# Optimization experiments

Hardware: AMD Instinct MI355X
Metric: run time of the kernel (lower is better)

## Reference

```python
import jax, jax.numpy as jnp
import numpy as np

EPS = 1e-5

def _conv_bn_relu(x, w, gamma, beta):
    # x: [B, C, N], w: [O, C] (1x1 conv, no bias)
    y = jnp.einsum('oc,bcn->bon', w, x)
    # BatchNorm1d in training mode: per-channel stats over (B, N)
    mean = jnp.mean(y, axis=(0, 2), keepdims=True)
    var = jnp.var(y, axis=(0, 2), keepdims=True)
    yhat = (y - mean) * jax.lax.rsqrt(var + EPS)
    return jax.nn.relu(gamma[None, :, None] * yhat + beta[None, :, None])


def setup_inputs() -> dict:
    key = jax.random.key(0)
    ks = jax.random.split(key, 8)
    B, C, N, Cr = 4, 256, 4096, 32
    x = jax.random.normal(ks[0], (B, C, N), dtype=jnp.float32)
    w1 = jax.random.normal(ks[1], (Cr, C), dtype=jnp.float32) * (1.0 / np.sqrt(C))
    w2 = jax.random.normal(ks[2], (Cr, C), dtype=jnp.float32) * (1.0 / np.sqrt(C))
    w3 = jax.random.normal(ks[3], (C, C), dtype=jnp.float32) * (1.0 / np.sqrt(C))
    g1 = 1.0 + 0.1 * jax.random.normal(ks[4], (Cr,), dtype=jnp.float32)
    b1 = 0.1 * jax.random.normal(ks[5], (Cr,), dtype=jnp.float32)
    g2 = 1.0 + 0.1 * jax.random.normal(ks[6], (Cr,), dtype=jnp.float32)
    b2 = 0.1 * jax.random.normal(ks[7], (Cr,), dtype=jnp.float32)
    g3 = jnp.ones((C,), dtype=jnp.float32)
    b3 = jnp.zeros((C,), dtype=jnp.float32)
    return {'x': x, 'w1': w1, 'w2': w2, 'w3': w3,
            'g1': g1, 'b1': b1, 'g2': g2, 'b2': b2, 'g3': g3, 'b3': b3}


def reference(x, w1, w2, w3, g1, b1, g2, b2, g3, b3):
    # a: [B, N, Cr] (queries), k: [B, Cr, N] (keys)
    a = _conv_bn_relu(x, w1, g1, b1).transpose(0, 2, 1)
    k = _conv_bn_relu(x, w2, g2, b2)
    # s[b, n, m] = softmax_m(sum_c a[b,n,c] * k[b,c,m])
    s = jax.nn.softmax(jnp.einsum('bnc,bcm->bnm', a, k), axis=-1)
    d = _conv_bn_relu(x, w3, g3, b3)  # [B, C, N]
    # out = x + d @ s^T : out[b,c,m] = sum_n d[b,c,n] * s[m,n]
    out = x + jnp.einsum('bcn,bmn->bcm', d, s)
    return out
```

## Files before the change

### kernel.cpp

```cpp
#include <hip/hip_runtime.h>
#include <cstddef>
#include <cstdint>

#define B_ 4
#define C_ 256
#define N_ 4096
#define KF_OFF_B  ((size_t)1024 * 1024)
#define DF_OFF_B  ((size_t)2 * 1024 * 1024)
#define SUM_OFF_B ((size_t)10 * 1024 * 1024)
#define ML_OFF_B  (SUM_OFF_B + 1280 * 4)
#define XH_OFF_B  (ML_OFF_B + 524288)
#define XL_OFF_B  (XH_OFF_B + (size_t)8 * 1024 * 1024)
#define WH_OFF_B  (XL_OFF_B + (size_t)8 * 1024 * 1024)
#define WL_OFF_B  (WH_OFF_B + 163840)
#define LOG2E 1.4426950408889634f

typedef unsigned short bfraw;
typedef __attribute__((ext_vector_type(8))) short short8;
typedef __attribute__((ext_vector_type(4))) float float4v;
typedef __attribute__((ext_vector_type(4))) bfraw bfraw4;

__device__ inline bfraw f2bf(float f) {
    union { float f; uint32_t u; } c; c.f = f;
    uint32_t u = c.u;
    u += 0x7fffu + ((u >> 16) & 1u);
    return (bfraw)(u >> 16);
}
__device__ inline float bf2f(bfraw h) {
    union { uint32_t u; float f; } c; c.u = ((uint32_t)h) << 16;
    return c.f;
}
#if __has_builtin(__builtin_amdgcn_exp2f)
__device__ inline float EXP2(float x) { return __builtin_amdgcn_exp2f(x); }
#else
__device__ inline float EXP2(float x) { return exp2f(x); }
#endif
__device__ inline uint32_t pack2(float a, float b) {
    union { float f; uint32_t u; } ca, cb; ca.f = a; cb.f = b;
#if __has_builtin(__builtin_amdgcn_perm)
    return __builtin_amdgcn_perm(cb.u + 0x8000u, ca.u + 0x8000u, 0x07060302u);
#else
    return ((ca.u + 0x8000u) >> 16) | ((cb.u + 0x8000u) & 0xffff0000u);
#endif
}

__global__ __launch_bounds__(256) void prep_kernel(
    const float* __restrict__ x,
    const float* __restrict__ w1, const float* __restrict__ w2,
    const float* __restrict__ w3, uint8_t* __restrict__ wsb)
{
    __shared__ float Ls[64][65];
    if (blockIdx.x >= 1024) {
        int bid = blockIdx.x - 1024;
        if (bid == 0) {
            float* sums = (float*)(wsb + SUM_OFF_B);
            for (int i = threadIdx.x; i < 640; i += 256) sums[i] = 0.f;
        }
        bfraw* wh = (bfraw*)(wsb + WH_OFF_B);
        bfraw* wl = (bfraw*)(wsb + WL_OFF_B);
        int idx4 = (bid * 256 + threadIdx.x) * 4;
        int ch = idx4 >> 8, k = idx4 & 255;
        const float* wr = (ch < 32) ? (w1 + ch * C_)
                          : (ch < 64) ? (w2 + (ch - 32) * C_)
                                      : (w3 + (ch - 64) * C_);
        float4 v = *(const float4*)&wr[k];
        float va[4] = {v.x, v.y, v.z, v.w};
        bfraw4 h, l;
#pragma unroll
        for (int j = 0; j < 4; ++j) {
            h[j] = f2bf(va[j]);
            l[j] = f2bf(va[j] - bf2f(h[j]));
        }
        *(bfraw4*)&wh[idx4] = h;
        *(bfraw4*)&wl[idx4] = l;
        return;
    }
    bfraw* xh = (bfraw*)(wsb + XH_OFF_B);
    bfraw* xl = (bfraw*)(wsb + XL_OFF_B);
    const int id = blockIdx.x;
    const int b  = id >> 8;
    const int c0 = ((id >> 6) & 3) << 6;
    const int n0 = (id & 63) << 6;
    const int t  = threadIdx.x;
    {
        int cl = t >> 4, nc = (t & 15) << 2;
#pragma unroll
        for (int i = 0; i < 4; ++i) {
            float4 v = *(const float4*)&x[((size_t)b * C_ + c0 + cl + i * 16) * N_ + n0 + nc];
            Ls[cl + i * 16][nc + 0] = v.x;
            Ls[cl + i * 16][nc + 1] = v.y;
            Ls[cl + i * 16][nc + 2] = v.z;
            Ls[cl + i * 16][nc + 3] = v.w;
        }
    }
    __syncthreads();
    int nl = t >> 2, seg = t & 3;
    bfraw hb[16], lb[16];
#pragma unroll
    for (int j = 0; j < 16; ++j) {
        float v = Ls[seg * 16 + j][nl];
        bfraw h = f2bf(v);
        hb[j] = h;
        lb[j] = f2bf(v - bf2f(h));
    }
    size_t base = ((size_t)b * N_ + n0 + nl) * 256 + c0 + seg * 16;
    *(short8*)&xh[base]     = *(short8*)&hb[0];
    *(short8*)&xh[base + 8] = *(short8*)&hb[8];
    *(short8*)&xl[base]     = *(short8*)&lb[0];
    *(short8*)&xl[base + 8] = *(short8*)&lb[8];
}

__global__ __launch_bounds__(256, 2) void ygemm_kernel(uint8_t* __restrict__ wsb)
{
    const bfraw* xh = (const bfraw*)(wsb + XH_OFF_B);
    const bfraw* xl = (const bfraw*)(wsb + XL_OFF_B);
    const bfraw* wh = (const bfraw*)(wsb + WH_OFF_B);
    const bfraw* wl = (const bfraw*)(wsb + WL_OFF_B);
    bfraw* qf  = (bfraw*)wsb;
    bfraw* kfp = (bfraw*)(wsb + KF_OFF_B);
    bfraw* dfp = (bfraw*)(wsb + DF_OFF_B);
    float* sums  = (float*)(wsb + SUM_OFF_B);
    float* sumsq = sums + 320;
    __shared__ float redS[4][64], redQ[4][64];

    const int bx = blockIdx.x;
    const int by = blockIdx.y;
    const int b  = bx >> 5;
    const int n0 = (bx << 7) & (N_ - 1);
    const int t = threadIdx.x, w = t >> 6, l = t & 63, lq = l & 15, lg = l >> 4;
    const int nw = n0 + w * 32;

    float4v acc[4][2];
#pragma unroll
    for (int i = 0; i < 4; ++i)
#pragma unroll
        for (int j = 0; j < 2; ++j) acc[i][j] = (float4v){0.f, 0.f, 0.f, 0.f};

    for (int s = 0; s < 8; ++s) {
        const int k0 = s * 32;
        short8 ah[4], al[4], bh[2], bl[2];
#pragma unroll
        for (int ct = 0; ct < 4; ++ct) {
            size_t off = (size_t)(by * 64 + ct * 16 + lq) * 256 + k0 + lg * 8;
            ah[ct] = *(const short8*)&wh[off];
            al[ct] = *(const short8*)&wl[off];
        }
#pragma unroll
        for (int nt = 0; nt < 2; ++nt) {
            size_t off = ((size_t)b * N_ + nw + nt * 16 + lq) * 256 + k0 + lg * 8;
            bh[nt] = *(const short8*)&xh[off];
            bl[nt] = *(const short8*)&xl[off];
        }
#pragma unroll
        for (int ct = 0; ct < 4; ++ct)
#pragma unroll
            for (int nt = 0; nt < 2; ++nt) {
                acc[ct][nt] = __builtin_amdgcn_mfma_f32_16x16x32_bf16(ah[ct], bh[nt], acc[ct][nt], 0, 0, 0);
                acc[ct][nt] = __builtin_amdgcn_mfma_f32_16x16x32_bf16(al[ct], bh[nt], acc[ct][nt], 0, 0, 0);
                acc[ct][nt] = __builtin_amdgcn_mfma_f32_16x16x32_bf16(ah[ct], bl[nt], acc[ct][nt], 0, 0, 0);
            }
    }
#pragma unroll
    for (int ct = 0; ct < 4; ++ct) {
        float sv[4], qv[4];
#pragma unroll
        for (int r = 0; r < 4; ++r) {
            float a0 = acc[ct][0][r], a1 = acc[ct][1][r];
            sv[r] = a0 + a1;
            qv[r] = a0 * a0 + a1 * a1;
#pragma unroll
            for (int m = 1; m < 16; m <<= 1) {
                sv[r] += __shfl_xor(sv[r], m);
                qv[r] += __shfl_xor(qv[r], m);
            }
        }
        if (lq == 0) {
#pragma unroll
            for (int r = 0; r < 4; ++r) {
                redS[w][ct * 16 + lg * 4 + r] = sv[r];
                redQ[w][ct * 16 + lg * 4 + r] = qv[r];
            }
        }
    }
    __syncthreads();
    if (t < 64) {
        float s = redS[0][t] + redS[1][t] + redS[2][t] + redS[3][t];
        float q = redQ[0][t] + redQ[1][t] + redQ[2][t] + redQ[3][t];
        atomicAdd(&sums[by * 64 + t], s);
        atomicAdd(&sumsq[by * 64 + t], q);
    }
    if (by == 0) {
#pragma unroll
        for (int ct = 0; ct < 4; ++ct)
#pragma unroll
            for (int nt = 0; nt < 2; ++nt)
#pragma unroll
                for (int r = 0; r < 4; ++r) {
                    int c = ct * 16 + lg * 4 + r;
                    int n = nw + nt * 16 + lq;
                    size_t addr = ((size_t)(b << 8) + (n >> 4)) * 512
                                + (size_t)(((n & 15) | (((c >> 3) & 3) << 4)) << 3) + (c & 7);
                    bfraw v = f2bf(acc[ct][nt][r]);
                    if (c < 32) qf[addr] = v; else kfp[addr] = v;
                }
    } else {
#pragma unroll
        for (int ct = 0; ct < 4; ++ct)
#pragma unroll
            for (int nt = 0; nt < 2; ++nt)
#pragma unroll
                for (int r = 0; r < 4; ++r) {
                    int cg = (by - 1) * 64 + ct * 16 + lg * 4 + r;
                    int n = nw + nt * 16 + lq;
                    size_t addr = (((size_t)(b << 4) + (cg >> 4)) * 128 + (n >> 5)) * 512
                                + (size_t)(((cg & 15) | (((n >> 3) & 3) << 4)) << 3) + (n & 7);
                    dfp[addr] = f2bf(acc[ct][nt][r]);
                }
    }
}

__device__ inline void bn_coef(const float* __restrict__ sums,
                               const float* __restrict__ g1, const float* __restrict__ b1,
                               const float* __restrict__ g2, const float* __restrict__ b2,
                               const float* __restrict__ g3, const float* __restrict__ b3,
                               int ch, float& sc, float& bi)
{
    const float inv = 1.0f / (float)(B_ * N_);
    float mean = sums[ch] * inv;
    float var  = sums[320 + ch] * inv - mean * mean;
    float g, bb;
    if (ch < 32)      { g = g1[ch];      bb = b1[ch]; }
    else if (ch < 64) { g = g2[ch - 32]; bb = b2[ch - 32]; }
    else              { g = g3[ch - 64]; bb = b3[ch - 64]; }
    sc = g * rsqrtf(var + 1e-5f);
    bi = bb - sc * mean;
    if (ch < 32) { sc *= LOG2E; bi *= LOG2E; }
}

__global__ __launch_bounds__(256) void affine_kernel(
    uint8_t* __restrict__ wsb,
    const float* __restrict__ g1, const float* __restrict__ b1,
    const float* __restrict__ g2, const float* __restrict__ b2,
    const float* __restrict__ g3, const float* __restrict__ b3)
{
    bfraw* base = (bfraw*)wsb;
    const float* sums = (const float*)(wsb + SUM_OFF_B);
    size_t i8 = ((size_t)blockIdx.x * 256 + threadIdx.x) * 8;
    bfraw4 v0 = *(bfraw4*)&base[i8];
    bfraw4 v1 = *(bfraw4*)&base[i8 + 4];
    if (i8 < 1048576) {
        int ch0 = (((int)(i8 >> 7)) & 3) * 8 + ((i8 < 524288) ? 0 : 32);
        float sa[8], ca[8];
#pragma unroll
        for (int j = 0; j < 8; ++j)
            bn_coef(sums, g1, b1, g2, b2, g3, b3, ch0 + j, sa[j], ca[j]);
#pragma unroll
        for (int j = 0; j < 4; ++j) {
            v0[j] = f2bf(fmaxf(0.f, fmaf(sa[j],     bf2f(v0[j]), ca[j])));
            v1[j] = f2bf(fmaxf(0.f, fmaf(sa[j + 4], bf2f(v1[j]), ca[j + 4])));
        }
    } else {
        size_t rel = i8 - 1048576;
        int ch = 64 + (((int)(rel >> 16)) & 15) * 16 + (((int)(rel >> 3)) & 15);
        float s, b;
        bn_coef(sums, g1, b1, g2, b2, g3, b3, ch, s, b);
#pragma unroll
        for (int j = 0; j < 4; ++j) {
            v0[j] = f2bf(fmaxf(0.f, fmaf(s, bf2f(v0[j]), b)));
            v1[j] = f2bf(fmaxf(0.f, fmaf(s, bf2f(v1[j]), b)));
        }
    }
    *(bfraw4*)&base[i8] = v0;
    *(bfraw4*)&base[i8 + 4] = v1;
}

__global__ __launch_bounds__(512, 2) void flash_kernel(
    const float* __restrict__ x, const uint8_t* __restrict__ wsb,
    float* __restrict__ out)
{
    const bfraw* qf  = (const bfraw*)wsb;
    const bfraw* kfp = (const bfraw*)(wsb + KF_OFF_B);
    const bfraw* dfp = (const bfraw*)(wsb + DF_OFF_B);
    __shared__ bfraw Pl[2][64 * 128];
    __shared__ bfraw kst[2][8 * 512];
    __shared__ float mfac[2][2][64];
    __shared__ uint2 flagw[2];
    __shared__ float msh[2][64], lsh[2][64];

    const int id  = blockIdx.x;
    const int b   = id & 3;
    const int n0q = (id >> 2) << 6;
    const int tid = threadIdx.x;
    const int w   = tid >> 6;
    const int l   = tid & 63;
    const int lq  = l & 15;
    const int lg  = l >> 4;
    const int sw  = lq & 7;
    const int qt_s   = w >> 1;
    const int ks_loc = w & 1;
    const int ctg0 = w;
    const int ctg1 = 8 + w;

    const short8 qfrag = *(const short8*)&qf[((size_t)(b * 256 + (n0q >> 4) + qt_s)) * 512 + l * 8];

    float m = 0.f, ps = 0.f;
    float4v zv = {0.f, 0.f, 0.f, 0.f};

    float4v accA[2][4], accB[2][4];
#pragma unroll
    for (int i = 0; i < 2; ++i)
#pragma unroll
        for (int j = 0; j < 4; ++j) {
            accA[i][j] = (float4v){0.f, 0.f, 0.f, 0.f};
            accB[i][j] = (float4v){0.f, 0.f, 0.f, 0.f};
        }

    short8 dfr[2][4];
#pragma unroll
    for (int ch = 0; ch < 4; ++ch) {
        dfr[0][ch] = *(const short8*)&dfp[(((size_t)(b * 16 + ctg0)) * 128 + ch) * 512 + l * 8];
        dfr[1][ch] = *(const short8*)&dfp[(((size_t)(b * 16 + ctg1)) * 128 + ch) * 512 + l * 8];
    }
    {
        short8 v = *(const short8*)&kfp[((size_t)(b * 256 + w)) * 512 + l * 8];
        *(short8*)&kst[0][w * 512 + l * 8] = v;
    }
    __syncthreads();

    const int qrow = qt_s * 16 + lq;
    for (int it = 0; it < 32; ++it) {
        const int ib = it & 1;
        const int nit = (it + 1) & 31;
        short8 kstage = *(const short8*)&kfp[((size_t)(b * 256 + nit * 8 + w)) * 512 + l * 8];
        short8 kfr[4];
#pragma unroll
        for (int kt = 0; kt < 4; ++kt)
            kfr[kt] = *(const short8*)&kst[ib][(ks_loc * 4 + kt) * 512 + l * 8];
        float4v st[4];
#pragma unroll
        for (int kt = 0; kt < 4; ++kt)
            st[kt] = __builtin_amdgcn_mfma_f32_16x16x32_bf16(kfr[kt], qfrag, zv, 0, 0, 0);
        float pm = st[0][0];
#pragma unroll
        for (int kt = 0; kt < 4; ++kt)
#pragma unroll
            for (int r = 0; r < 4; ++r) pm = fmaxf(pm, st[kt][r]);
        pm = fmaxf(pm, __shfl_xor(pm, 16));
        pm = fmaxf(pm, __shfl_xor(pm, 32));
        const int resc = __any(pm > 8.0f);
        float f = 1.0f;
        if (resc) {
            float d = fmaxf(pm, 0.f);
            f = EXP2(-d);
            ps *= f;
#pragma unroll
            for (int kt = 0; kt < 4; ++kt)
#pragma unroll
                for (int r = 0; r < 4; ++r) st[kt][r] -= d;
            m += d;
#pragma unroll
            for (int r = 0; r < 4; ++r) zv[r] -= d;
        }
#pragma unroll
        for (int kt = 0; kt < 4; ++kt) {
            float e0 = EXP2(st[kt][0]);
            float e1 = EXP2(st[kt][1]);
            float e2 = EXP2(st[kt][2]);
            float e3 = EXP2(st[kt][3]);
            ps += (e0 + e1) + (e2 + e3);
            uint2 pd = {pack2(e0, e1), pack2(e2, e3)};
            int g = (2 * (ks_loc * 4 + kt) + (lg >> 1)) ^ sw;
            *(uint2*)&Pl[ib][qrow * 128 + g * 8 + (lg & 1) * 4] = pd;
        }
        if (lg == 0) mfac[ib][ks_loc][qrow] = f;
        if (l == 0) ((unsigned char*)&flagw[ib])[ks_loc * 4 + qt_s] = (unsigned char)resc;
        *(short8*)&kst[ib ^ 1][w * 512 + l * 8] = kstage;
        __syncthreads();
        uint2 fw = flagw[ib];
        if (fw.x | fw.y) {
            float fA[4], fB[4];
#pragma unroll
            for (int j = 0; j < 4; ++j) {
                fA[j] = mfac[ib][0][j * 16 + lq];
                fB[j] = mfac[ib][1][j * 16 + lq];
            }
#pragma unroll
            for (int ct = 0; ct < 2; ++ct)
#pragma unroll
                for (int j = 0; j < 4; ++j)
#pragma unroll
                    for (int r = 0; r < 4; ++r) {
                        accA[ct][j][r] *= fA[j];
                        accB[ct][j][r] *= fB[j];
                    }
        }
#pragma unroll
        for (int ch = 0; ch < 4; ++ch) {
            short8 bfr[4];
            int g = (ch * 4 + lg) ^ sw;
#pragma unroll
            for (int qt = 0; qt < 4; ++qt)
                bfr[qt] = *(const short8*)&Pl[ib][(qt * 16 + lq) * 128 + g * 8];
            __builtin_amdgcn_s_setprio(1);
            if (ch < 2) {
#pragma unroll
                for (int qt = 0; qt < 4; ++qt) {
                    accA[0][qt] = __builtin_amdgcn_mfma_f32_16x16x32_bf16(dfr[0][ch], bfr[qt], accA[0][qt], 0, 0, 0);
                    accA[1][qt] = __builtin_amdgcn_mfma_f32_16x16x32_bf16(dfr[1][ch], bfr[qt], accA[1][qt], 0, 0, 0);
                }
            } else {
#pragma unroll
                for (int qt = 0; qt < 4; ++qt) {
                    accB[0][qt] = __builtin_amdgcn_mfma_f32_16x16x32_bf16(dfr[0][ch], bfr[qt], accB[0][qt], 0, 0, 0);
                    accB[1][qt] = __builtin_amdgcn_mfma_f32_16x16x32_bf16(dfr[1][ch], bfr[qt], accB[1][qt], 0, 0, 0);
                }
            }
            __builtin_amdgcn_s_setprio(0);
            dfr[0][ch] = *(const short8*)&dfp[(((size_t)(b * 16 + ctg0)) * 128 + nit * 4 + ch) * 512 + l * 8];
            dfr[1][ch] = *(const short8*)&dfp[(((size_t)(b * 16 + ctg1)) * 128 + nit * 4 + ch) * 512 + l * 8];
        }
    }
    ps += __shfl_xor(ps, 16);
    ps += __shfl_xor(ps, 32);
    if (lg == 0) { msh[ks_loc][qrow] = m; lsh[ks_loc][qrow] = ps; }
    __syncthreads();
    float rA[4], rB[4];
#pragma unroll
    for (int qt = 0; qt < 4; ++qt) {
        float m0 = msh[0][qt * 16 + lq], m1 = msh[1][qt * 16 + lq];
        float l0 = lsh[0][qt * 16 + lq], l1 = lsh[1][qt * 16 + lq];
        float M = fmaxf(m0, m1);
        float sA = EXP2(m0 - M), sB = EXP2(m1 - M);
        float inv = 1.0f / (l0 * sA + l1 * sB);
        rA[qt] = sA * inv;
        rB[qt] = sB * inv;
    }
#pragma unroll
    for (int ct = 0; ct < 2; ++ct) {
        int ctg = ct ? ctg1 : ctg0;
#pragma unroll
        for (int r = 0; r < 4; ++r) {
            int c = ctg * 16 + lg * 4 + r;
            size_t base = ((size_t)b * C_ + c) * N_ + n0q;
#pragma unroll
            for (int qt = 0; qt < 4; ++qt) {
                size_t idx = base + qt * 16 + lq;
                out[idx] = x[idx] + accA[ct][qt][r] * rA[qt] + accB[ct][qt][r] * rB[qt];
            }
        }
    }
}

extern "C" void kernel_launch(void* const* d_in, const int* in_sizes, int n_in,
                              void* d_out, int out_size, void* d_ws, size_t ws_size,
                              hipStream_t stream) {
    (void)in_sizes; (void)n_in; (void)out_size; (void)ws_size;
    const float* x  = (const float*)d_in[0];
    const float* w1 = (const float*)d_in[1];
    const float* w2 = (const float*)d_in[2];
    const float* w3 = (const float*)d_in[3];
    const float* g1 = (const float*)d_in[4];
    const float* b1 = (const float*)d_in[5];
    const float* g2 = (const float*)d_in[6];
    const float* b2 = (const float*)d_in[7];
    const float* g3 = (const float*)d_in[8];
    const float* b3 = (const float*)d_in[9];
    uint8_t* wsb = (uint8_t*)d_ws;
    float* outp = (float*)d_out;

    prep_kernel<<<1104, 256, 0, stream>>>(x, w1, w2, w3, wsb);
    ygemm_kernel<<<dim3(128, 5), 256, 0, stream>>>(wsb);
    affine_kernel<<<2560, 256, 0, stream>>>(wsb, g1, b1, g2, b2, g3, b3);
    flash_kernel<<<256, 512, 0, stream>>>(x, wsb, outp);
}
```

Baseline: 184.5 us.

## Halve query tile to 32 rows, split keys four ways, double flash grid

The flash kernel now handles 32 queries per block instead of 64 and launches 512 blocks instead of 256. Within a block the eight waves are split as 2 query tiles times 4 key-slice groups, each keeping its own running scale, and the four partial softmax states are merged at the end. Launch bounds are raised to allow four blocks per CU. The aim is to fill more of the CUs and raise occupancy, at the cost of loading K and D tiles twice as often per query and a slightly more complex final merge.

```diff
diff --git a/kernel.cpp b/kernel.cpp
--- a/kernel.cpp
+++ b/kernel.cpp
@@ -274,30 +274,31 @@
     *(bfraw4*)&base[i8 + 4] = v1;
 }
 
-__global__ __launch_bounds__(512, 2) void flash_kernel(
+__global__ __launch_bounds__(512, 4) void flash_kernel(
     const float* __restrict__ x, const uint8_t* __restrict__ wsb,
     float* __restrict__ out)
 {
     const bfraw* qf  = (const bfraw*)wsb;
     const bfraw* kfp = (const bfraw*)(wsb + KF_OFF_B);
     const bfraw* dfp = (const bfraw*)(wsb + DF_OFF_B);
-    __shared__ bfraw Pl[2][64 * 128];
+    __shared__ bfraw Pl[2][32 * 128];
     __shared__ bfraw kst[2][8 * 512];
-    __shared__ float mfac[2][2][64];
+    __shared__ float mfac[2][4][32];
     __shared__ uint2 flagw[2];
-    __shared__ float msh[2][64], lsh[2][64];
+    __shared__ float msh[4][32], lsh[4][32];
 
     const int id  = blockIdx.x;
-    const int b   = id & 3;
-    const int n0q = (id >> 2) << 6;
+    const int b   = (id >> 1) & 3;
+    const int qb  = ((id >> 3) << 1) | (id & 1);
+    const int n0q = qb << 5;
     const int tid = threadIdx.x;
     const int w   = tid >> 6;
     const int l   = tid & 63;
     const int lq  = l & 15;
     const int lg  = l >> 4;
     const int sw  = lq & 7;
-    const int qt_s   = w >> 1;
-    const int ks_loc = w & 1;
+    const int qt_s = w >> 2;
+    const int kq   = w & 3;
     const int ctg0 = w;
     const int ctg1 = 8 + w;
 
@@ -306,14 +307,13 @@
     float m = 0.f, ps = 0.f;
     float4v zv = {0.f, 0.f, 0.f, 0.f};
 
-    float4v accA[2][4], accB[2][4];
-#pragma unroll
-    for (int i = 0; i < 2; ++i)
-#pragma unroll
-        for (int j = 0; j < 4; ++j) {
-            accA[i][j] = (float4v){0.f, 0.f, 0.f, 0.f};
-            accB[i][j] = (float4v){0.f, 0.f, 0.f, 0.f};
-        }
+    float4v accQ[4][2][2];
+#pragma unroll
+    for (int i = 0; i < 4; ++i)
+#pragma unroll
+        for (int j = 0; j < 2; ++j)
+#pragma unroll
+            for (int k = 0; k < 2; ++k) accQ[i][j][k] = (float4v){0.f, 0.f, 0.f, 0.f};
 
     short8 dfr[2][4];
 #pragma unroll
@@ -332,19 +332,16 @@
         const int ib = it & 1;
         const int nit = (it + 1) & 31;
         short8 kstage = *(const short8*)&kfp[((size_t)(b * 256 + nit * 8 + w)) * 512 + l * 8];
-        short8 kfr[4];
-#pragma unroll
-        for (int kt = 0; kt < 4; ++kt)
-            kfr[kt] = *(const short8*)&kst[ib][(ks_loc * 4 + kt) * 512 + l * 8];
-        float4v st[4];
-#pragma unroll
-        for (int kt = 0; kt < 4; ++kt)
+        short8 kfr[2];
+#pragma unroll
+        for (int kt = 0; kt < 2; ++kt)
+            kfr[kt] = *(const short8*)&kst[ib][(kq * 2 + kt) * 512 + l * 8];
+        float4v st[2];
+#pragma unroll
+        for (int kt = 0; kt < 2; ++kt)
             st[kt] = __builtin_amdgcn_mfma_f32_16x16x32_bf16(kfr[kt], qfrag, zv, 0, 0, 0);
-        float pm = st[0][0];
-#pragma unroll
-        for (int kt = 0; kt < 4; ++kt)
-#pragma unroll
-            for (int r = 0; r < 4; ++r) pm = fmaxf(pm, st[kt][r]);
+        float pm = fmaxf(fmaxf(fmaxf(st[0][0], st[0][1]), fmaxf(st[0][2], st[0][3])),
+                         fmaxf(fmaxf(st[1][0], st[1][1]), fmaxf(st[1][2], st[1][3])));
         pm = fmaxf(pm, __shfl_xor(pm, 16));
         pm = fmaxf(pm, __shfl_xor(pm, 32));
         const int resc = __any(pm > 8.0f);
@@ -354,7 +351,7 @@
             f = EXP2(-d);
             ps *= f;
 #pragma unroll
-            for (int kt = 0; kt < 4; ++kt)
+            for (int kt = 0; kt < 2; ++kt)
 #pragma unroll
                 for (int r = 0; r < 4; ++r) st[kt][r] -= d;
             m += d;
@@ -362,58 +359,50 @@
             for (int r = 0; r < 4; ++r) zv[r] -= d;
         }
 #pragma unroll
-        for (int kt = 0; kt < 4; ++kt) {
+        for (int kt = 0; kt < 2; ++kt) {
             float e0 = EXP2(st[kt][0]);
             float e1 = EXP2(st[kt][1]);
             float e2 = EXP2(st[kt][2]);
             float e3 = EXP2(st[kt][3]);
             ps += (e0 + e1) + (e2 + e3);
             uint2 pd = {pack2(e0, e1), pack2(e2, e3)};
-            int g = (2 * (ks_loc * 4 + kt) + (lg >> 1)) ^ sw;
+            int g = (kq * 4 + kt * 2 + (lg >> 1)) ^ sw;
             *(uint2*)&Pl[ib][qrow * 128 + g * 8 + (lg & 1) * 4] = pd;
         }
-        if (lg == 0) mfac[ib][ks_loc][qrow] = f;
-        if (l == 0) ((unsigned char*)&flagw[ib])[ks_loc * 4 + qt_s] = (unsigned char)resc;
+        if (lg == 0) mfac[ib][kq][qrow] = f;
+        if (l == 0) ((unsigned char*)&flagw[ib])[kq * 2 + qt_s] = (unsigned char)resc;
         *(short8*)&kst[ib ^ 1][w * 512 + l * 8] = kstage;
         __syncthreads();
         uint2 fw = flagw[ib];
         if (fw.x | fw.y) {
-            float fA[4], fB[4];
-#pragma unroll
-            for (int j = 0; j < 4; ++j) {
-                fA[j] = mfac[ib][0][j * 16 + lq];
-                fB[j] = mfac[ib][1][j * 16 + lq];
-            }
-#pragma unroll
-            for (int ct = 0; ct < 2; ++ct)
-#pragma unroll
-                for (int j = 0; j < 4; ++j)
-#pragma unroll
-                    for (int r = 0; r < 4; ++r) {
-                        accA[ct][j][r] *= fA[j];
-                        accB[ct][j][r] *= fB[j];
-                    }
+            float fq[4][2];
+#pragma unroll
+            for (int j = 0; j < 4; ++j)
+#pragma unroll
+                for (int qt = 0; qt < 2; ++qt)
+                    fq[j][qt] = mfac[ib][j][qt * 16 + lq];
+#pragma unroll
+            for (int j = 0; j < 4; ++j)
+#pragma unroll
+                for (int ct = 0; ct < 2; ++ct)
+#pragma unroll
+                    for (int qt = 0; qt < 2; ++qt)
+#pragma unroll
+                        for (int r = 0; r < 4; ++r)
+                            accQ[j][ct][qt][r] *= fq[j][qt];
         }
 #pragma unroll
         for (int ch = 0; ch < 4; ++ch) {
-            short8 bfr[4];
+            short8 bfr[2];
             int g = (ch * 4 + lg) ^ sw;
 #pragma unroll
-            for (int qt = 0; qt < 4; ++qt)
+            for (int qt = 0; qt < 2; ++qt)
                 bfr[qt] = *(const short8*)&Pl[ib][(qt * 16 + lq) * 128 + g * 8];
             __builtin_amdgcn_s_setprio(1);
-            if (ch < 2) {
-#pragma unroll
-                for (int qt = 0; qt < 4; ++qt) {
-                    accA[0][qt] = __builtin_amdgcn_mfma_f32_16x16x32_bf16(dfr[0][ch], bfr[qt], accA[0][qt], 0, 0, 0);
-                    accA[1][qt] = __builtin_amdgcn_mfma_f32_16x16x32_bf16(dfr[1][ch], bfr[qt], accA[1][qt], 0, 0, 0);
-                }
-            } else {
-#pragma unroll
-                for (int qt = 0; qt < 4; ++qt) {
-                    accB[0][qt] = __builtin_amdgcn_mfma_f32_16x16x32_bf16(dfr[0][ch], bfr[qt], accB[0][qt], 0, 0, 0);
-                    accB[1][qt] = __builtin_amdgcn_mfma_f32_16x16x32_bf16(dfr[1][ch], bfr[qt], accB[1][qt], 0, 0, 0);
-                }
+#pragma unroll
+            for (int qt = 0; qt < 2; ++qt) {
+                accQ[ch][0][qt] = __builtin_amdgcn_mfma_f32_16x16x32_bf16(dfr[0][ch], bfr[qt], accQ[ch][0][qt], 0, 0, 0);
+                accQ[ch][1][qt] = __builtin_amdgcn_mfma_f32_16x16x32_bf16(dfr[1][ch], bfr[qt], accQ[ch][1][qt], 0, 0, 0);
             }
             __builtin_amdgcn_s_setprio(0);
             dfr[0][ch] = *(const short8*)&dfp[(((size_t)(b * 16 + ctg0)) * 128 + nit * 4 + ch) * 512 + l * 8];
@@ -422,18 +411,27 @@
     }
     ps += __shfl_xor(ps, 16);
     ps += __shfl_xor(ps, 32);
-    if (lg == 0) { msh[ks_loc][qrow] = m; lsh[ks_loc][qrow] = ps; }
+    if (lg == 0) { msh[kq][qrow] = m; lsh[kq][qrow] = ps; }
     __syncthreads();
-    float rA[4], rB[4];
-#pragma unroll
-    for (int qt = 0; qt < 4; ++qt) {
-        float m0 = msh[0][qt * 16 + lq], m1 = msh[1][qt * 16 + lq];
-        float l0 = lsh[0][qt * 16 + lq], l1 = lsh[1][qt * 16 + lq];
-        float M = fmaxf(m0, m1);
-        float sA = EXP2(m0 - M), sB = EXP2(m1 - M);
-        float inv = 1.0f / (l0 * sA + l1 * sB);
-        rA[qt] = sA * inv;
-        rB[qt] = sB * inv;
+    float rz[2][4];
+#pragma unroll
+    for (int qt = 0; qt < 2; ++qt) {
+        float mv[4], lv[4];
+#pragma unroll
+        for (int j = 0; j < 4; ++j) {
+            mv[j] = msh[j][qt * 16 + lq];
+            lv[j] = lsh[j][qt * 16 + lq];
+        }
+        float M = fmaxf(fmaxf(mv[0], mv[1]), fmaxf(mv[2], mv[3]));
+        float den = 0.f;
+#pragma unroll
+        for (int j = 0; j < 4; ++j) {
+            rz[qt][j] = EXP2(mv[j] - M);
+            den += lv[j] * rz[qt][j];
+        }
+        float inv = 1.0f / den;
+#pragma unroll
+        for (int j = 0; j < 4; ++j) rz[qt][j] *= inv;
     }
 #pragma unroll
     for (int ct = 0; ct < 2; ++ct) {
@@ -443,9 +441,11 @@
             int c = ctg * 16 + lg * 4 + r;
             size_t base = ((size_t)b * C_ + c) * N_ + n0q;
 #pragma unroll
-            for (int qt = 0; qt < 4; ++qt) {
+            for (int qt = 0; qt < 2; ++qt) {
                 size_t idx = base + qt * 16 + lq;
-                out[idx] = x[idx] + accA[ct][qt][r] * rA[qt] + accB[ct][qt][r] * rB[qt];
+                float o = accQ[0][ct][qt][r] * rz[qt][0] + accQ[1][ct][qt][r] * rz[qt][1]
+                        + accQ[2][ct][qt][r] * rz[qt][2] + accQ[3][ct][qt][r] * rz[qt][3];
+                out[idx] = x[idx] + o;
             }
         }
     }
@@ -471,5 +471,5 @@
     prep_kernel<<<1104, 256, 0, stream>>>(x, w1, w2, w3, wsb);
     ygemm_kernel<<<dim3(128, 5), 256, 0, stream>>>(wsb);
     affine_kernel<<<2560, 256, 0, stream>>>(wsb, g1, b1, g2, b2, g3, b3);
-    flash_kernel<<<256, 512, 0, stream>>>(x, wsb, outp);
-}
+    flash_kernel<<<512, 512, 0, stream>>>(x, wsb, outp);
+}
```

Measured after the change: 247.1 us. 33.9% more time.
